# Kernel tuning notes

Hardware: AMD Instinct MI355X
Metric: run time of the kernel (lower is better)

## Reference

```python
import jax, jax.numpy as jnp
import numpy as np

B, T, D, H = 2, 2048, 1024, 16
HD = D // H  # head_size = 64
EPS = 1e-5


def _layernorm(x, g, b):
    mu = jnp.mean(x, axis=-1, keepdims=True)
    var = jnp.mean(jnp.square(x - mu), axis=-1, keepdims=True)
    return (x - mu) * jax.lax.rsqrt(var + EPS) * g + b


def setup_inputs() -> dict:
    key = jax.random.key(0)
    ks = jax.random.split(key, 16)
    s = 0.02
    return {
        "x": jax.random.normal(ks[0], (B, T, D), jnp.float32),
        # per-head Q/K/V linears, stacked over heads: [H, D, HD] (in,out layout)
        "wq": jax.random.normal(ks[1], (H, D, HD), jnp.float32) * s,
        "bq": jnp.zeros((H, HD), jnp.float32),
        "wk": jax.random.normal(ks[2], (H, D, HD), jnp.float32) * s,
        "bk": jnp.zeros((H, HD), jnp.float32),
        "wv": jax.random.normal(ks[3], (H, D, HD), jnp.float32) * s,
        "bv": jnp.zeros((H, HD), jnp.float32),
        "wp": jax.random.normal(ks[4], (D, D), jnp.float32) * s,
        "bp": jnp.zeros((D,), jnp.float32),
        "w1": jax.random.normal(ks[5], (D, 4 * D), jnp.float32) * s,
        "b1": jnp.zeros((4 * D,), jnp.float32),
        "w2": jax.random.normal(ks[6], (4 * D, D), jnp.float32) * s,
        "b2": jnp.zeros((D,), jnp.float32),
        "ln1_g": jnp.ones((D,), jnp.float32),
        "ln1_b": jnp.zeros((D,), jnp.float32),
        "lnf_g": jnp.ones((D,), jnp.float32),
        "lnf_b": jnp.zeros((D,), jnp.float32),
        "ln2_g": jnp.ones((D,), jnp.float32),
        "ln2_b": jnp.zeros((D,), jnp.float32),
    }


def reference(x, wq, bq, wk, bk, wv, bv, wp, bp, w1, b1, w2, b2,
              ln1_g, ln1_b, lnf_g, lnf_b, ln2_g, ln2_b):
    b_, t_, d_ = x.shape
    # batched per-head projections: [B,H,T,HD]
    Q = jnp.einsum('btd,hde->bhte', x, wq) + bq[None, :, None, :]
    K = jnp.einsum('btd,hde->bhte', x, wk) + bk[None, :, None, :]
    V = jnp.einsum('btd,hde->bhte', x, wv) + bv[None, :, None, :]
    # raw attention scores, scaled -- NOTE: no softmax, no mask (matches source)
    wei = jnp.einsum('bhte,bhse->bhts', Q, K) * (HD ** -0.5)
    attn = jnp.einsum('bhts,bhse->bhte', wei, V)  # [B,H,T,HD]
    # concat heads along last dim == [B,T,H*HD]
    cat = attn.transpose(0, 2, 1, 3).reshape(b_, t_, d_)
    Kc = K.transpose(0, 2, 1, 3).reshape(b_, t_, d_)
    Vc = V.transpose(0, 2, 1, 3).reshape(b_, t_, d_)
    out = cat @ wp + bp
    out1 = _layernorm(x + out, ln1_g, ln1_b)
    # FeedForward: ln(idx + net(idx)) internally
    ff = jax.nn.relu(out1 @ w1 + b1) @ w2 + b2
    ffo = _layernorm(out1 + ff, lnf_g, lnf_b)
    out2 = _layernorm(out1 + ffo, ln2_g, ln2_b)
    return (out2, Kc, Vc)
```

## Files before the change

### kernel.cpp

```cpp
#include <hip/hip_runtime.h>

typedef unsigned short u16;
typedef __attribute__((ext_vector_type(4))) float f32x4;
typedef __attribute__((ext_vector_type(8))) __bf16 bf16x8;
typedef __attribute__((ext_vector_type(8))) unsigned short u16x8;
typedef __attribute__((ext_vector_type(4))) unsigned short u16x4;

__device__ __forceinline__ u16 f2b(float f) {
    unsigned int u = __builtin_bit_cast(unsigned int, f);
    u = (u + 0x7FFFu + ((u >> 16) & 1u)) >> 16;
    return (u16)u;
}
__device__ __forceinline__ float b2f(u16 h) {
    unsigned int u = ((unsigned int)h) << 16;
    return __builtin_bit_cast(float, u);
}

__device__ __forceinline__ void gload_lds16(const u16* g, u16* l) {
    __builtin_amdgcn_global_load_lds(
        (const __attribute__((address_space(1))) void*)g,
        (__attribute__((address_space(3))) void*)l,
        16, 0, 0);
}

__device__ __forceinline__ bf16x8 lds_frag(const u16* p) {
    u16x8 t = *(const u16x8*)p;
    return __builtin_bit_cast(bf16x8, t);
}

#define FENCE asm volatile("" ::: "memory")
#define BARRIER do { FENCE; __builtin_amdgcn_s_barrier(); FENCE; \
                     __builtin_amdgcn_sched_barrier(0); } while (0)
#define LGKM0 do { asm volatile("s_waitcnt lgkmcnt(0)" ::: "memory"); \
                   __builtin_amdgcn_sched_barrier(0); } while (0)
#define WAIT_VM8 do { asm volatile("s_waitcnt vmcnt(8)" ::: "memory"); \
                      __builtin_amdgcn_sched_barrier(0); } while (0)
#define WAIT_VM4 do { asm volatile("s_waitcnt vmcnt(4)" ::: "memory"); \
                      __builtin_amdgcn_sched_barrier(0); } while (0)
#define WAIT_VM0 do { asm volatile("s_waitcnt vmcnt(0)" ::: "memory"); \
                      __builtin_amdgcn_sched_barrier(0); } while (0)

__global__ __launch_bounds__(256) void cast_x_kernel(const float* __restrict__ in,
                                                     u16* __restrict__ out) {
    int i = (blockIdx.x * 256 + threadIdx.x) * 4;
    float4 v = *(const float4*)&in[i];
    u16x4 o = { f2b(v.x), f2b(v.y), f2b(v.z), f2b(v.w) };
    *(u16x4*)&out[i] = o;
}

__global__ __launch_bounds__(256) void tr_wqkv(const float* __restrict__ wq,
                                               const float* __restrict__ wk,
                                               const float* __restrict__ wv,
                                               u16* __restrict__ WT) {
    __shared__ float tile[32][33];
    int z = blockIdx.z;
    int sel = z >> 4, h = z & 15;
    const float* w = (sel == 0) ? wq : (sel == 1) ? wk : wv;
    w += (long)h * 65536;
    int tx = threadIdx.x & 31, ty = threadIdx.x >> 5;
    int d0 = blockIdx.x * 32, e0 = blockIdx.y * 32;
#pragma unroll
    for (int i = 0; i < 32; i += 8)
        tile[ty + i][tx] = w[(long)(d0 + ty + i) * 64 + e0 + tx];
    __syncthreads();
#pragma unroll
    for (int i = 0; i < 32; i += 8)
        WT[((long)(sel * 1024 + h * 64 + e0 + ty + i)) * 1024 + d0 + tx] = f2b(tile[tx][ty + i]);
}

__global__ __launch_bounds__(256) void prep_bias(const float* __restrict__ bq,
                                                 const float* __restrict__ bk,
                                                 const float* __restrict__ bv,
                                                 float* __restrict__ BI) {
    int i = blockIdx.x * 256 + threadIdx.x;
    const float* b = (i < 1024) ? bq : (i < 2048) ? bk : bv;
    BI[i] = b[((i & 1023) >> 6) * 64 + (i & 63)];
}

__global__ __launch_bounds__(256) void transpose_cast(const float* __restrict__ in,
                                                      u16* __restrict__ out, int R, int C) {
    __shared__ float tile[32][33];
    int tx = threadIdx.x & 31, ty = threadIdx.x >> 5;
    int r0 = blockIdx.y * 32, c0 = blockIdx.x * 32;
#pragma unroll
    for (int i = 0; i < 32; i += 8)
        tile[ty + i][tx] = in[(long)(r0 + ty + i) * C + c0 + tx];
    __syncthreads();
#pragma unroll
    for (int i = 0; i < 32; i += 8)
        out[(long)(c0 + ty + i) * R + r0 + tx] = f2b(tile[tx][ty + i]);
}

#define PHASEX(Sa, Sb, mh, kh, LOADB, STAGE_STMT, WAIT_STMT) do {             \
    if (LOADB) {                                                              \
        _Pragma("unroll") for (int n = 0; n < NF; ++n)                        \
            bfr[n] = lds_frag(&(Sb)[((brow0 + (n << 4)) << 6) +               \
                                    (eoff ^ ((kh) * 32))]);                   \
    }                                                                         \
    _Pragma("unroll") for (int m4 = 0; m4 < MFH; ++m4)                        \
        af[m4] = lds_frag(&(Sa)[((arow0 + (((mh) * MFH + m4) << 4)) << 6) +   \
                                (eoff ^ ((kh) * 32))]);                       \
    STAGE_STMT;                                                               \
    BARRIER;                                                                  \
    LGKM0;                                                                    \
    __builtin_amdgcn_s_setprio(1);                                            \
    _Pragma("unroll") for (int m4 = 0; m4 < MFH; ++m4)                        \
        _Pragma("unroll") for (int n = 0; n < NF; ++n)                        \
            acc[(mh) * MFH + m4][n] = __builtin_amdgcn_mfma_f32_16x16x32_bf16(\
                af[m4], bfr[n], acc[(mh) * MFH + m4][n], 0, 0, 0);            \
    __builtin_amdgcn_s_setprio(0);                                            \
    WAIT_STMT;                                                                \
    BARRIER;                                                                  \
} while (0)

template <int MODE, int WM, int WN, int MF, int NF, int MSPLIT>
__global__ __launch_bounds__(WM * WN * 64, 2) void gemmT(
    const u16* __restrict__ A, const u16* __restrict__ BT, const float* __restrict__ bias,
    u16* __restrict__ Cb, float* __restrict__ KV,
    u16* __restrict__ Q0, u16* __restrict__ Q1,
    int M, int N, int K, int lda, int ldb, int ldc, int kchunk) {
    constexpr int T   = WM * WN * 64;
    constexpr int BM  = WM * MF * 16;
    constexpr int BN  = WN * NF * 16;
    constexpr int RPI = T / 8;
    constexpr int LA  = BM / RPI;
    constexpr int LB  = BN / RPI;
    constexpr int EPI = T * 8;
    constexpr int MFH = MF / MSPLIT;
    __shared__ __align__(16) u16 As[2][BM * 64];
    __shared__ __align__(16) u16 Bs[2][BN * 64];
    const int tid = threadIdx.x;
    const int lane = tid & 63;
    const int wid = tid >> 6;
    const int wr = wid / WN, wc = wid % WN;
    const int ntile = N / BN;
    int bid = blockIdx.x;
    int kb = 0, ksz = K;
    u16* Pout = Q0;
    if (MODE == 4) {
        int tiles = (M / BM) * ntile;
        int sk = bid / tiles; bid -= sk * tiles;
        kb = sk * kchunk;
        int rem = K - kb; ksz = rem < kchunk ? rem : kchunk;
        Pout = sk ? Q1 : Q0;
    }
    const int bi = bid / ntile, bj = bid % ntile;
    const int brow = bi * BM, bcol = bj * BN;
    const int nt = ksz >> 6;
    const int niter = nt >> 1;

    const int srow = tid >> 3;
    const int scol = ((tid & 7) ^ (srow & 7)) << 3;
    const u16* ag = A + (long)(brow + srow) * lda + kb + scol;
    const u16* bg = BT + (long)(bcol + srow) * ldb + kb + scol;
    const long aI = (long)RPI * lda, bI = (long)RPI * ldb;
    const int sdst = tid << 3;

    auto STG = [&](int buf, int t, int half) {
#pragma unroll
        for (int j = 0; j < LA / 2; ++j)
            gload_lds16(ag + ((long)t << 6) + (half * (LA / 2) + j) * aI,
                        &As[buf][(half * (LA / 2) + j) * EPI + sdst]);
#pragma unroll
        for (int j = 0; j < LB / 2; ++j)
            gload_lds16(bg + ((long)t << 6) + (half * (LB / 2) + j) * bI,
                        &Bs[buf][(half * (LB / 2) + j) * EPI + sdst]);
    };

    f32x4 acc[MF][NF] = {};

    const int ln15 = lane & 15;
    const int eoff = (((lane >> 4) << 3) ^ ((lane & 7) << 3));
    const int arow0 = wr * (MF * 16) + ln15;
    const int brow0 = wc * (NF * 16) + ln15;

    STG(0, 0, 0); STG(0, 0, 1);
    if (nt > 1) { STG(1, 1, 0); STG(1, 1, 1); WAIT_VM8; }
    else WAIT_VM0;
    BARRIER;

    for (int I = 0; I < niter; ++I) {
        const int t0 = 2 * I;
        const bool hn0 = (t0 + 2 < nt);
        const bool hn1 = (t0 + 3 < nt);
        const bool notlast = (I + 1 < niter);
        bf16x8 af[MFH], bfr[NF];
        if constexpr (MSPLIT == 2) {
            PHASEX(As[0], Bs[0], 0, 0, true,  { if (I > 0) STG(1, t0 + 1, 1); }, {});
            PHASEX(As[0], Bs[0], 1, 0, false, {}, {});
            PHASEX(As[0], Bs[0], 0, 1, true,  {}, {});
            PHASEX(As[0], Bs[0], 1, 1, false, { if (hn0) STG(0, t0 + 2, 0); },
                   { if (hn0) WAIT_VM4; else WAIT_VM0; });
            PHASEX(As[1], Bs[1], 0, 0, true,  { if (hn0) STG(0, t0 + 2, 1); }, {});
            PHASEX(As[1], Bs[1], 1, 0, false, {}, {});
            PHASEX(As[1], Bs[1], 0, 1, true,  {}, {});
            PHASEX(As[1], Bs[1], 1, 1, false, { if (hn1) STG(1, t0 + 3, 0); },
                   { if (notlast) { if (hn1) WAIT_VM4; else WAIT_VM0; } });
        } else {
            PHASEX(As[0], Bs[0], 0, 0, true,  { if (I > 0) STG(1, t0 + 1, 1); }, {});
            PHASEX(As[0], Bs[0], 0, 1, true,  { if (hn0) STG(0, t0 + 2, 0); },
                   { if (hn0) WAIT_VM4; else WAIT_VM0; });
            PHASEX(As[1], Bs[1], 0, 0, true,  { if (hn0) STG(0, t0 + 2, 1); }, {});
            PHASEX(As[1], Bs[1], 0, 1, true,  { if (hn1) STG(1, t0 + 3, 0); },
                   { if (notlast) { if (hn1) WAIT_VM4; else WAIT_VM0; } });
        }
    }

#pragma unroll
    for (int m = 0; m < MF; ++m) {
        int row = brow + wr * (MF * 16) + (m << 4) + ((lane >> 4) << 2);
#pragma unroll
        for (int n = 0; n < NF; ++n) {
            int col = bcol + wc * (NF * 16) + (n << 4) + ln15;
            float bv = (MODE == 4) ? 0.f : bias[col];
#pragma unroll
            for (int r = 0; r < 4; ++r) {
                float v = acc[m][n][r] + bv;
                long off = (long)(row + r) * ldc + col;
                if (MODE == 2) { v = v > 0.f ? v : 0.f; Cb[off] = f2b(v); }
                if (MODE == 1) {
                    Cb[off] = f2b(v);
                    if (col >= 1024) {
                        int c = col - 1024;
                        KV[(long)(c >> 10) * 4194304 + (long)(row + r) * 1024 + (c & 1023)] = v;
                    }
                }
                if (MODE == 4) Pout[off] = f2b(v);
            }
        }
    }
}

__global__ __launch_bounds__(256) void ktv_partial(const u16* __restrict__ QKVB,
                                                   float* __restrict__ KTVF) {
    __shared__ __align__(16) u16 Ks[64 * 64];
    __shared__ __align__(16) u16 Vs[64 * 64];
    int tid = threadIdx.x;
    int tc = blockIdx.x, bh = blockIdx.y;
    int b = bh >> 4, h = bh & 15;
    int j = tid & 63, i0 = (tid >> 6) * 16;
    float acc[16] = {};
    for (int st = 0; st < 4; ++st) {
        int t0 = tc * 256 + st * 64;
        __syncthreads();
#pragma unroll
        for (int i = 0; i < 2; ++i) {
            int c = i * 256 + tid;
            long base = (long)(b * 2048 + t0 + (c >> 3)) * 3072 + h * 64 + (c & 7) * 8;
            *(u16x8*)&Ks[c * 8] = *(const u16x8*)&QKVB[base + 1024];
            *(u16x8*)&Vs[c * 8] = *(const u16x8*)&QKVB[base + 2048];
        }
        __syncthreads();
        for (int tt = 0; tt < 64; ++tt) {
            float vj = b2f(Vs[tt * 64 + j]);
            u16x8 k0 = *(const u16x8*)&Ks[tt * 64 + i0];
            u16x8 k1 = *(const u16x8*)&Ks[tt * 64 + i0 + 8];
#pragma unroll
            for (int r = 0; r < 8; ++r) acc[r] += b2f(k0[r]) * vj;
#pragma unroll
            for (int r = 0; r < 8; ++r) acc[r + 8] += b2f(k1[r]) * vj;
        }
    }
#pragma unroll
    for (int r = 0; r < 16; ++r)
        atomicAdd(&KTVF[bh * 4096 + (i0 + r) * 64 + j], acc[r]);
}

__global__ __launch_bounds__(256) void cast_ktv(const float* __restrict__ KTVF,
                                                u16* __restrict__ KTVT) {
    int idx = blockIdx.x * 256 + threadIdx.x;
    int bh = idx >> 12, r = idx & 4095;
    int n = r >> 6, k = r & 63;
    KTVT[idx] = f2b(KTVF[bh * 4096 + k * 64 + n] * 0.125f);
}

__global__ __launch_bounds__(256) void attn_gemm(const u16* __restrict__ QKVB,
                                                 const u16* __restrict__ KTVT,
                                                 u16* __restrict__ cat) {
    __shared__ __align__(16) u16 Qs[64 * 64];
    __shared__ __align__(16) u16 Bs[64 * 64];
    int tid = threadIdx.x, wid = tid >> 6, lane = tid & 63;
    int rt = blockIdx.x, bh = blockIdx.y;
    int b = bh >> 4, h = bh & 15;
    long qbase = (long)(b * 2048 + rt * 64) * 3072 + h * 64;
#pragma unroll
    for (int i = 0; i < 2; ++i) {
        int c = i * 256 + tid;
        gload_lds16(QKVB + qbase + (c >> 3) * 3072 + (c & 7) * 8, &Qs[(i * 256 + wid * 64) * 8]);
        gload_lds16(KTVT + bh * 4096 + c * 8, &Bs[(i * 256 + wid * 64) * 8]);
    }
    __syncthreads();
    f32x4 acc[4] = {};
#pragma unroll
    for (int kk = 0; kk < 2; ++kk) {
        bf16x8 a = lds_frag(&Qs[(wid * 16 + (lane & 15)) * 64 + kk * 32 + (lane >> 4) * 8]);
#pragma unroll
        for (int n = 0; n < 4; ++n) {
            bf16x8 bb = lds_frag(&Bs[(n * 16 + (lane & 15)) * 64 + kk * 32 + (lane >> 4) * 8]);
            acc[n] = __builtin_amdgcn_mfma_f32_16x16x32_bf16(a, bb, acc[n], 0, 0, 0);
        }
    }
#pragma unroll
    for (int n = 0; n < 4; ++n)
#pragma unroll
        for (int r = 0; r < 4; ++r) {
            int row = rt * 64 + wid * 16 + (lane >> 4) * 4 + r;
            int col = h * 64 + n * 16 + (lane & 15);
            cat[(long)(b * 2048 + row) * 1024 + col] = f2b(acc[n][r]);
        }
}

__device__ __forceinline__ void block_reduce2(float& a, float& b) {
    __syncthreads();
#pragma unroll
    for (int off = 32; off; off >>= 1) {
        a += __shfl_down(a, off);
        b += __shfl_down(b, off);
    }
    __shared__ float sa[4], sb[4];
    int wid = threadIdx.x >> 6, lane = threadIdx.x & 63;
    if (lane == 0) { sa[wid] = a; sb[wid] = b; }
    __syncthreads();
    a = sa[0] + sa[1] + sa[2] + sa[3];
    b = sb[0] + sb[1] + sb[2] + sb[3];
}

__global__ __launch_bounds__(256) void ln1_kernel(
    const float* __restrict__ x,
    const u16* __restrict__ q0, const u16* __restrict__ q1,
    const float* __restrict__ bp,
    const float* __restrict__ g, const float* __restrict__ bt,
    float* __restrict__ out1f, u16* __restrict__ out1b) {
    int row = blockIdx.x, tid = threadIdx.x;
    long base = (long)row * 1024 + tid * 4;
    float4 xv = *(const float4*)&x[base];
    u16x4 a0 = *(const u16x4*)&q0[base];
    u16x4 a1 = *(const u16x4*)&q1[base];
    float4 bb = *(const float4*)&bp[tid * 4];
    float xa[4] = { xv.x, xv.y, xv.z, xv.w };
    float bba[4] = { bb.x, bb.y, bb.z, bb.w };
    float s[4];
#pragma unroll
    for (int r = 0; r < 4; ++r)
        s[r] = xa[r] + b2f(a0[r]) + b2f(a1[r]) + bba[r];
    float sum = s[0] + s[1] + s[2] + s[3];
    float sq = s[0] * s[0] + s[1] * s[1] + s[2] * s[2] + s[3] * s[3];
    block_reduce2(sum, sq);
    float mu = sum * (1.f / 1024.f);
    float var = sq * (1.f / 1024.f) - mu * mu;
    float rs = rsqrtf(var + 1e-5f);
    float o0 = (s[0] - mu) * rs * g[tid * 4 + 0] + bt[tid * 4 + 0];
    float o1 = (s[1] - mu) * rs * g[tid * 4 + 1] + bt[tid * 4 + 1];
    float o2 = (s[2] - mu) * rs * g[tid * 4 + 2] + bt[tid * 4 + 2];
    float o3 = (s[3] - mu) * rs * g[tid * 4 + 3] + bt[tid * 4 + 3];
    float4 of; of.x = o0; of.y = o1; of.z = o2; of.w = o3;
    u16x4 ob = (u16x4){ f2b(o0), f2b(o1), f2b(o2), f2b(o3) };
    *(float4*)&out1f[base] = of;
    *(u16x4*)&out1b[base] = ob;
}

__global__ __launch_bounds__(256) void lnf_kernel(
    const float* __restrict__ out1f,
    const u16* __restrict__ q0, const u16* __restrict__ q1,
    const float* __restrict__ b2,
    const float* __restrict__ lnfg, const float* __restrict__ lnfb,
    const float* __restrict__ ln2g, const float* __restrict__ ln2b,
    float* __restrict__ out2) {
    int row = blockIdx.x, tid = threadIdx.x;
    long base = (long)row * 1024 + tid * 4;
    float4 o1 = *(const float4*)&out1f[base];
    u16x4 a0 = *(const u16x4*)&q0[base];
    u16x4 a1 = *(const u16x4*)&q1[base];
    float4 bb = *(const float4*)&b2[tid * 4];
    float o1a[4] = { o1.x, o1.y, o1.z, o1.w };
    float bba[4] = { bb.x, bb.y, bb.z, bb.w };
    float s1[4];
#pragma unroll
    for (int r = 0; r < 4; ++r)
        s1[r] = o1a[r] + b2f(a0[r]) + b2f(a1[r]) + bba[r];
    float sum = s1[0] + s1[1] + s1[2] + s1[3];
    float sq = s1[0] * s1[0] + s1[1] * s1[1] + s1[2] * s1[2] + s1[3] * s1[3];
    block_reduce2(sum, sq);
    float mu = sum * (1.f / 1024.f);
    float rs = rsqrtf(sq * (1.f / 1024.f) - mu * mu + 1e-5f);
    float s2[4];
#pragma unroll
    for (int r = 0; r < 4; ++r) {
        float ffo = (s1[r] - mu) * rs * lnfg[tid * 4 + r] + lnfb[tid * 4 + r];
        s2[r] = o1a[r] + ffo;
    }
    float sum2 = s2[0] + s2[1] + s2[2] + s2[3];
    float sq2 = s2[0] * s2[0] + s2[1] * s2[1] + s2[2] * s2[2] + s2[3] * s2[3];
    block_reduce2(sum2, sq2);
    float mu2 = sum2 * (1.f / 1024.f);
    float rs2 = rsqrtf(sq2 * (1.f / 1024.f) - mu2 * mu2 + 1e-5f);
    float4 o;
    o.x = (s2[0] - mu2) * rs2 * ln2g[tid * 4 + 0] + ln2b[tid * 4 + 0];
    o.y = (s2[1] - mu2) * rs2 * ln2g[tid * 4 + 1] + ln2b[tid * 4 + 1];
    o.z = (s2[2] - mu2) * rs2 * ln2g[tid * 4 + 2] + ln2b[tid * 4 + 2];
    o.w = (s2[3] - mu2) * rs2 * ln2g[tid * 4 + 3] + ln2b[tid * 4 + 3];
    *(float4*)&out2[base] = o;
}

extern "C" void kernel_launch(void* const* d_in, const int* in_sizes, int n_in,
                              void* d_out, int out_size, void* d_ws, size_t ws_size,
                              hipStream_t stream) {
    const float* x    = (const float*)d_in[0];
    const float* wq   = (const float*)d_in[1];
    const float* bq   = (const float*)d_in[2];
    const float* wk   = (const float*)d_in[3];
    const float* bk   = (const float*)d_in[4];
    const float* wv   = (const float*)d_in[5];
    const float* bv   = (const float*)d_in[6];
    const float* wp   = (const float*)d_in[7];
    const float* bp   = (const float*)d_in[8];
    const float* w1   = (const float*)d_in[9];
    const float* b1   = (const float*)d_in[10];
    const float* w2   = (const float*)d_in[11];
    const float* b2   = (const float*)d_in[12];
    const float* ln1g = (const float*)d_in[13];
    const float* ln1b = (const float*)d_in[14];
    const float* lnfg = (const float*)d_in[15];
    const float* lnfb = (const float*)d_in[16];
    const float* ln2g = (const float*)d_in[17];
    const float* ln2b = (const float*)d_in[18];

    float* out2 = (float*)d_out;
    float* kv   = (float*)d_out + 4194304;

    char* ws = (char*)d_ws;
    u16*   XB     = (u16*)  (ws + 0);
    u16*   CAT    = XB;
    u16*   WQKVT  = (u16*)  (ws + 8388608);
    float* BQKV   = (float*)(ws + 14680064);
    u16*   WPT    = (u16*)  (ws + 14692352);
    u16*   W1T    = (u16*)  (ws + 16789504);
    u16*   W2T    = (u16*)  (ws + 25178112);
    float* KTVF   = (float*)(ws + 33566720);
    u16*   KTVT   = (u16*)  (ws + 34091008);
    u16*   QKVB   = (u16*)  (ws + 34353152);
    u16*   OUT1B  = QKVB;
    u16*   Q3_0   = (u16*)  (ws + 59518976);
    u16*   Q3_1   = (u16*)  (ws + 67907584);
    float* OUT1F  = (float*)(ws + 76296192);
    u16*   H1     = (u16*)  (ws + 93073408);
    u16*   Q5_0   = (u16*)  (ws + 0);
    u16*   Q5_1   = (u16*)  (ws + 34353152);
    (void)ws_size; (void)in_sizes; (void)n_in; (void)out_size;

    hipMemsetAsync(KTVF, 0, 32 * 4096 * 4, stream);
    cast_x_kernel<<<4096, 256, 0, stream>>>(x, XB);
    tr_wqkv<<<dim3(32, 2, 48), 256, 0, stream>>>(wq, wk, wv, WQKVT);
    prep_bias<<<12, 256, 0, stream>>>(bq, bk, bv, BQKV);
    transpose_cast<<<dim3(32, 32), 256, 0, stream>>>(wp, WPT, 1024, 1024);
    transpose_cast<<<dim3(128, 32), 256, 0, stream>>>(w1, W1T, 1024, 4096);
    transpose_cast<<<dim3(32, 128), 256, 0, stream>>>(w2, W2T, 4096, 1024);

    gemmT<1, 2, 4, 4, 6, 2><<<256, 512, 0, stream>>>(
        XB, WQKVT, BQKV, QKVB, kv, nullptr, nullptr,
        4096, 3072, 1024, 1024, 1024, 3072, 0);
    ktv_partial<<<dim3(8, 32), 256, 0, stream>>>(QKVB, KTVF);
    cast_ktv<<<512, 256, 0, stream>>>(KTVF, KTVT);
    attn_gemm<<<dim3(32, 32), 256, 0, stream>>>(QKVB, KTVT, CAT);

    gemmT<4, 2, 2, 4, 4, 1><<<512, 256, 0, stream>>>(
        CAT, WPT, nullptr, nullptr, nullptr, Q3_0, Q3_1,
        4096, 1024, 1024, 1024, 1024, 1024, 512);
    ln1_kernel<<<4096, 256, 0, stream>>>(x, Q3_0, Q3_1, bp, ln1g, ln1b, OUT1F, OUT1B);

    gemmT<2, 2, 4, 8, 4, 2><<<256, 512, 0, stream>>>(
        OUT1B, W1T, b1, H1, nullptr, nullptr, nullptr,
        4096, 4096, 1024, 1024, 1024, 4096, 0);
    gemmT<4, 2, 2, 4, 4, 1><<<512, 256, 0, stream>>>(
        H1, W2T, nullptr, nullptr, nullptr, Q5_0, Q5_1,
        4096, 1024, 4096, 4096, 4096, 1024, 2048);
    lnf_kernel<<<4096, 256, 0, stream>>>(OUT1F, Q5_0, Q5_1, b2,
                                         lnfg, lnfb, ln2g, ln2b, out2);
}
```

Measured before the change: 224.2 us.

## Stage GEMM epilogue through LDS, swizzle tile order, split K/V fp32 export

The GEMM epilogue now writes bf16 results into shared memory and then stores them to global memory in coalesced 16-byte chunks, replacing scattered 2-byte stores. Block indices are remapped so consecutive groups of blocks traverse tiles column-major with an 8-way interleave, aiming at better L2/XCD locality. The fp32 K/V output is no longer written from the QKV GEMM epilogue; a separate kernel expands it from the bf16 QKV buffer. This adds a kernel launch and rounds K/V outputs through bf16, which reduces their precision.

```diff
diff --git a/kernel.cpp b/kernel.cpp
--- a/kernel.cpp
+++ b/kernel.cpp
@@ -89,6 +89,19 @@
 #pragma unroll
     for (int i = 0; i < 32; i += 8)
         out[(long)(c0 + ty + i) * R + r0 + tx] = f2b(tile[tx][ty + i]);
+}
+
+__global__ __launch_bounds__(256) void kv_expand(const u16* __restrict__ QKVB,
+                                                 float* __restrict__ kv) {
+    int idx = blockIdx.x * 256 + threadIdx.x;
+    int row = idx >> 8;
+    int co = (idx & 255) * 8;
+    u16x8 v = *(const u16x8*)&QKVB[(long)row * 3072 + 1024 + co];
+    float4 f0 = { b2f(v[0]), b2f(v[1]), b2f(v[2]), b2f(v[3]) };
+    float4 f1 = { b2f(v[4]), b2f(v[5]), b2f(v[6]), b2f(v[7]) };
+    long base = (long)(co >> 10) * 4194304 + (long)row * 1024 + (co & 1023);
+    *(float4*)&kv[base] = f0;
+    *(float4*)&kv[base + 4] = f1;
 }
 
 #define PHASEX(Sa, Sb, mh, kh, LOADB, STAGE_STMT, WAIT_STMT) do {             \
@@ -116,8 +129,7 @@
 template <int MODE, int WM, int WN, int MF, int NF, int MSPLIT>
 __global__ __launch_bounds__(WM * WN * 64, 2) void gemmT(
     const u16* __restrict__ A, const u16* __restrict__ BT, const float* __restrict__ bias,
-    u16* __restrict__ Cb, float* __restrict__ KV,
-    u16* __restrict__ Q0, u16* __restrict__ Q1,
+    u16* __restrict__ Cb, u16* __restrict__ Q0, u16* __restrict__ Q1,
     int M, int N, int K, int lda, int ldb, int ldc, int kchunk) {
     constexpr int T   = WM * WN * 64;
     constexpr int BM  = WM * MF * 16;
@@ -127,24 +139,33 @@
     constexpr int LB  = BN / RPI;
     constexpr int EPI = T * 8;
     constexpr int MFH = MF / MSPLIT;
-    __shared__ __align__(16) u16 As[2][BM * 64];
-    __shared__ __align__(16) u16 Bs[2][BN * 64];
+    constexpr int ASZ = BM * 64, BSZ = BN * 64;
+    __shared__ __align__(16) u16 SMEM[2 * ASZ + 2 * BSZ];
+    u16* As0 = SMEM;
+    u16* As1 = SMEM + ASZ;
+    u16* Bs0 = SMEM + 2 * ASZ;
+    u16* Bs1 = SMEM + 2 * ASZ + BSZ;
     const int tid = threadIdx.x;
     const int lane = tid & 63;
     const int wid = tid >> 6;
     const int wr = wid / WN, wc = wid % WN;
     const int ntile = N / BN;
+    const int mtile = M / BM;
     int bid = blockIdx.x;
     int kb = 0, ksz = K;
     u16* Pout = Q0;
     if (MODE == 4) {
-        int tiles = (M / BM) * ntile;
+        int tiles = mtile * ntile;
         int sk = bid / tiles; bid -= sk * tiles;
         kb = sk * kchunk;
         int rem = K - kb; ksz = rem < kchunk ? rem : kchunk;
         Pout = sk ? Q1 : Q0;
     }
-    const int bi = bid / ntile, bj = bid % ntile;
+    {
+        int q = (mtile * ntile) >> 3;
+        bid = (bid & 7) * q + (bid >> 3);
+    }
+    const int bj = bid / mtile, bi = bid % mtile;
     const int brow = bi * BM, bcol = bj * BN;
     const int nt = ksz >> 6;
     const int niter = nt >> 1;
@@ -156,15 +177,15 @@
     const long aI = (long)RPI * lda, bI = (long)RPI * ldb;
     const int sdst = tid << 3;
 
-    auto STG = [&](int buf, int t, int half) {
+    auto STG = [&](u16* lA, u16* lB, int t, int half) {
 #pragma unroll
         for (int j = 0; j < LA / 2; ++j)
             gload_lds16(ag + ((long)t << 6) + (half * (LA / 2) + j) * aI,
-                        &As[buf][(half * (LA / 2) + j) * EPI + sdst]);
+                        &lA[(half * (LA / 2) + j) * EPI + sdst]);
 #pragma unroll
         for (int j = 0; j < LB / 2; ++j)
             gload_lds16(bg + ((long)t << 6) + (half * (LB / 2) + j) * bI,
-                        &Bs[buf][(half * (LB / 2) + j) * EPI + sdst]);
+                        &lB[(half * (LB / 2) + j) * EPI + sdst]);
     };
 
     f32x4 acc[MF][NF] = {};
@@ -174,8 +195,8 @@
     const int arow0 = wr * (MF * 16) + ln15;
     const int brow0 = wc * (NF * 16) + ln15;
 
-    STG(0, 0, 0); STG(0, 0, 1);
-    if (nt > 1) { STG(1, 1, 0); STG(1, 1, 1); WAIT_VM8; }
+    STG(As0, Bs0, 0, 0); STG(As0, Bs0, 0, 1);
+    if (nt > 1) { STG(As1, Bs1, 1, 0); STG(As1, Bs1, 1, 1); WAIT_VM8; }
     else WAIT_VM0;
     BARRIER;
 
@@ -186,48 +207,52 @@
         const bool notlast = (I + 1 < niter);
         bf16x8 af[MFH], bfr[NF];
         if constexpr (MSPLIT == 2) {
-            PHASEX(As[0], Bs[0], 0, 0, true,  { if (I > 0) STG(1, t0 + 1, 1); }, {});
-            PHASEX(As[0], Bs[0], 1, 0, false, {}, {});
-            PHASEX(As[0], Bs[0], 0, 1, true,  {}, {});
-            PHASEX(As[0], Bs[0], 1, 1, false, { if (hn0) STG(0, t0 + 2, 0); },
+            PHASEX(As0, Bs0, 0, 0, true,  { if (I > 0) STG(As1, Bs1, t0 + 1, 1); }, {});
+            PHASEX(As0, Bs0, 1, 0, false, {}, {});
+            PHASEX(As0, Bs0, 0, 1, true,  {}, {});
+            PHASEX(As0, Bs0, 1, 1, false, { if (hn0) STG(As0, Bs0, t0 + 2, 0); },
                    { if (hn0) WAIT_VM4; else WAIT_VM0; });
-            PHASEX(As[1], Bs[1], 0, 0, true,  { if (hn0) STG(0, t0 + 2, 1); }, {});
-            PHASEX(As[1], Bs[1], 1, 0, false, {}, {});
-            PHASEX(As[1], Bs[1], 0, 1, true,  {}, {});
-            PHASEX(As[1], Bs[1], 1, 1, false, { if (hn1) STG(1, t0 + 3, 0); },
+            PHASEX(As1, Bs1, 0, 0, true,  { if (hn0) STG(As0, Bs0, t0 + 2, 1); }, {});
+            PHASEX(As1, Bs1, 1, 0, false, {}, {});
+            PHASEX(As1, Bs1, 0, 1, true,  {}, {});
+            PHASEX(As1, Bs1, 1, 1, false, { if (hn1) STG(As1, Bs1, t0 + 3, 0); },
                    { if (notlast) { if (hn1) WAIT_VM4; else WAIT_VM0; } });
         } else {
-            PHASEX(As[0], Bs[0], 0, 0, true,  { if (I > 0) STG(1, t0 + 1, 1); }, {});
-            PHASEX(As[0], Bs[0], 0, 1, true,  { if (hn0) STG(0, t0 + 2, 0); },
+            PHASEX(As0, Bs0, 0, 0, true,  { if (I > 0) STG(As1, Bs1, t0 + 1, 1); }, {});
+            PHASEX(As0, Bs0, 0, 1, true,  { if (hn0) STG(As0, Bs0, t0 + 2, 0); },
                    { if (hn0) WAIT_VM4; else WAIT_VM0; });
-            PHASEX(As[1], Bs[1], 0, 0, true,  { if (hn0) STG(0, t0 + 2, 1); }, {});
-            PHASEX(As[1], Bs[1], 0, 1, true,  { if (hn1) STG(1, t0 + 3, 0); },
+            PHASEX(As1, Bs1, 0, 0, true,  { if (hn0) STG(As0, Bs0, t0 + 2, 1); }, {});
+            PHASEX(As1, Bs1, 0, 1, true,  { if (hn1) STG(As1, Bs1, t0 + 3, 0); },
                    { if (notlast) { if (hn1) WAIT_VM4; else WAIT_VM0; } });
         }
     }
 
+    const int crow0 = wr * (MF * 16), ccol0 = wc * (NF * 16);
 #pragma unroll
     for (int m = 0; m < MF; ++m) {
-        int row = brow + wr * (MF * 16) + (m << 4) + ((lane >> 4) << 2);
+        int rbase = crow0 + (m << 4) + ((lane >> 4) << 2);
 #pragma unroll
         for (int n = 0; n < NF; ++n) {
-            int col = bcol + wc * (NF * 16) + (n << 4) + ln15;
-            float bv = (MODE == 4) ? 0.f : bias[col];
+            int col = ccol0 + (n << 4) + ln15;
+            float bv = (MODE == 4) ? 0.f : bias[bcol + col];
 #pragma unroll
             for (int r = 0; r < 4; ++r) {
                 float v = acc[m][n][r] + bv;
-                long off = (long)(row + r) * ldc + col;
-                if (MODE == 2) { v = v > 0.f ? v : 0.f; Cb[off] = f2b(v); }
-                if (MODE == 1) {
-                    Cb[off] = f2b(v);
-                    if (col >= 1024) {
-                        int c = col - 1024;
-                        KV[(long)(c >> 10) * 4194304 + (long)(row + r) * 1024 + (c & 1023)] = v;
-                    }
-                }
-                if (MODE == 4) Pout[off] = f2b(v);
+                if (MODE == 2) v = v > 0.f ? v : 0.f;
+                SMEM[(rbase + r) * BN + col] = f2b(v);
             }
         }
+    }
+    LGKM0;
+    BARRIER;
+    u16* outp = (MODE == 4) ? Pout : Cb;
+    constexpr int CHT = BM * BN / 8 / T;
+#pragma unroll
+    for (int k = 0; k < CHT; ++k) {
+        int c = tid + k * T;
+        int row = c / (BN / 8), co = (c % (BN / 8)) * 8;
+        u16x8 vv = *(const u16x8*)&SMEM[row * BN + co];
+        *(u16x8*)&outp[(long)(brow + row) * ldc + bcol + co] = vv;
     }
 }
 
@@ -457,22 +482,23 @@
     transpose_cast<<<dim3(32, 128), 256, 0, stream>>>(w2, W2T, 4096, 1024);
 
     gemmT<1, 2, 4, 4, 6, 2><<<256, 512, 0, stream>>>(
-        XB, WQKVT, BQKV, QKVB, kv, nullptr, nullptr,
+        XB, WQKVT, BQKV, QKVB, nullptr, nullptr,
         4096, 3072, 1024, 1024, 1024, 3072, 0);
+    kv_expand<<<4096, 256, 0, stream>>>(QKVB, kv);
     ktv_partial<<<dim3(8, 32), 256, 0, stream>>>(QKVB, KTVF);
     cast_ktv<<<512, 256, 0, stream>>>(KTVF, KTVT);
     attn_gemm<<<dim3(32, 32), 256, 0, stream>>>(QKVB, KTVT, CAT);
 
     gemmT<4, 2, 2, 4, 4, 1><<<512, 256, 0, stream>>>(
-        CAT, WPT, nullptr, nullptr, nullptr, Q3_0, Q3_1,
+        CAT, WPT, nullptr, nullptr, Q3_0, Q3_1,
         4096, 1024, 1024, 1024, 1024, 1024, 512);
     ln1_kernel<<<4096, 256, 0, stream>>>(x, Q3_0, Q3_1, bp, ln1g, ln1b, OUT1F, OUT1B);
 
     gemmT<2, 2, 4, 8, 4, 2><<<256, 512, 0, stream>>>(
-        OUT1B, W1T, b1, H1, nullptr, nullptr, nullptr,
+        OUT1B, W1T, b1, H1, nullptr, nullptr,
         4096, 4096, 1024, 1024, 1024, 4096, 0);
     gemmT<4, 2, 2, 4, 4, 1><<<512, 256, 0, stream>>>(
-        H1, W2T, nullptr, nullptr, nullptr, Q5_0, Q5_1,
+        H1, W2T, nullptr, nullptr, Q5_0, Q5_1,
         4096, 1024, 4096, 4096, 4096, 1024, 2048);
     lnf_kernel<<<4096, 256, 0, stream>>>(OUT1F, Q5_0, Q5_1, b2,
                                          lnfg, lnfb, ln2g, ln2b, out2);
```

Result: no change. 220.5 us (-1.6%).
